# Kernel tuning notes

Measured on AMD Instinct MI355X. Metric: run time of the kernel, lower is better.

Reference implementation:

```python
import jax, jax.numpy as jnp
import numpy as np

EPS = 1e-5

def layernorm(x, g, b):
    mu = jnp.mean(x, axis=-1, keepdims=True)
    var = jnp.var(x, axis=-1, keepdims=True)
    return (x - mu) * jax.lax.rsqrt(var + EPS) * g + b

def setup_inputs() -> dict:
    key = jax.random.key(0)
    ks = jax.random.split(key, 12)
    B, T, C, H = 8, 2048, 64, 4
    d = C // H
    s = 0.02
    return {
        "x": jax.random.normal(ks[0], (B, T, C), jnp.float32),
        "Wq": jax.random.normal(ks[1], (H, C, d), jnp.float32) * s,
        "Wk": jax.random.normal(ks[2], (H, C, d), jnp.float32) * s,
        "Wv": jax.random.normal(ks[3], (H, C, d), jnp.float32) * s,
        "Wo": jax.random.normal(ks[4], (C, C), jnp.float32) * s,
        "bo": jnp.zeros((C,), jnp.float32),
        "W1": jax.random.normal(ks[5], (C, 4 * C), jnp.float32) * s,
        "bias1": jnp.zeros((4 * C,), jnp.float32),
        "W2": jax.random.normal(ks[6], (4 * C, C), jnp.float32) * s,
        "bias2": jnp.zeros((C,), jnp.float32),
        "gamma1": jnp.ones((C,), jnp.float32),
        "beta1": jnp.zeros((C,), jnp.float32),
        "gamma2": jnp.ones((C,), jnp.float32),
        "beta2": jnp.zeros((C,), jnp.float32),
    }

def reference(x, Wq, Wk, Wv, Wo, bo, W1, bias1, W2, bias2, gamma1, beta1, gamma2, beta2):
    B, T, C = x.shape
    H, _, d = Wq.shape
    # pre-LN attention
    h = layernorm(x, gamma1, beta1)
    q = jnp.einsum('btc,hcd->bhtd', h, Wq)
    k = jnp.einsum('btc,hcd->bhtd', h, Wk)
    v = jnp.einsum('btc,hcd->bhtd', h, Wv)
    scores = jnp.einsum('bhtd,bhsd->bhts', q, k) / jnp.sqrt(jnp.float32(d))
    causal = jnp.tril(jnp.ones((T, T), bool))
    scores = jnp.where(causal, scores, -jnp.inf)
    attn = jax.nn.softmax(scores, axis=-1)  # dropout = identity (eval)
    out = jnp.einsum('bhts,bhsd->bhtd', attn, v)
    out = out.transpose(0, 2, 1, 3).reshape(B, T, C)  # concat heads
    x = x + out @ Wo + bo
    # MLP
    h2 = layernorm(x, gamma2, beta2)
    x = x + jax.nn.relu(h2 @ W1 + bias1) @ W2 + bias2
    return x
```

## Files before the change

### kernel.cpp

```cpp
#include <hip/hip_runtime.h>

constexpr int Bn = 8, Tn = 2048;
constexpr int VS = 2080;

typedef __bf16 bf16x8 __attribute__((ext_vector_type(8)));
typedef float  f32x16 __attribute__((ext_vector_type(16)));
typedef short  short8 __attribute__((ext_vector_type(8)));
typedef unsigned short ushort_t;

__device__ __forceinline__ unsigned short f2bf(float f) {
    __bf16 h = (__bf16)f;
    return __builtin_bit_cast(unsigned short, h);
}

__device__ __forceinline__ float fast_exp2(float x) {
    float r;
    asm("v_exp_f32 %0, %1" : "=v"(r) : "v"(x));
    return r;
}

__device__ __forceinline__ unsigned cvt_pk_bf16(float lo, float hi_) {
    unsigned r;
    asm("v_cvt_pk_bf16_f32 %0, %1, %2" : "=v"(r) : "v"(lo), "v"(hi_));
    return r;
}

__device__ __forceinline__ bf16x8 xch_frag(
    float a0, float a1, float a2, float a3,
    float a4, float a5, float a6, float a7, int hi)
{
    const float s0 = hi ? a0 : a4, s1 = hi ? a1 : a5;
    const float s2 = hi ? a2 : a6, s3 = hi ? a3 : a7;
    const float r0 = __shfl_xor(s0, 32), r1 = __shfl_xor(s1, 32);
    const float r2 = __shfl_xor(s2, 32), r3 = __shfl_xor(s3, 32);
    bf16x8 f;
    f[0] = (__bf16)(hi ? r0 : a0); f[1] = (__bf16)(hi ? r1 : a1);
    f[2] = (__bf16)(hi ? r2 : a2); f[3] = (__bf16)(hi ? r3 : a3);
    f[4] = (__bf16)(hi ? a4 : r0); f[5] = (__bf16)(hi ? a5 : r1);
    f[6] = (__bf16)(hi ? a6 : r2); f[7] = (__bf16)(hi ? a7 : r3);
    return f;
}

__global__ __launch_bounds__(256) void k_prep(
    const float* __restrict__ Wo, const float* __restrict__ W1, const float* __restrict__ W2,
    const float* __restrict__ Wq, const float* __restrict__ Wk, const float* __restrict__ Wv,
    ushort_t* __restrict__ WoT, ushort_t* __restrict__ W1T, ushort_t* __restrict__ W2T,
    ushort_t* __restrict__ WqT, ushort_t* __restrict__ WkT, ushort_t* __restrict__ WvT,
    ushort_t* __restrict__ VT)
{
    const int i = blockIdx.x * 256 + threadIdx.x;
    if (i < 4096) {
        const int n = i >> 6, k = i & 63;
        WoT[i] = f2bf(Wo[k * 64 + n]);
    } else if (i < 20480) {
        const int i2 = i - 4096, n = i2 >> 6, k = i2 & 63;
        W1T[i2] = f2bf(W1[k * 256 + n]);
    } else if (i < 36864) {
        const int i2 = i - 20480, n = i2 >> 8, k = i2 & 255;
        W2T[i2] = f2bf(W2[k * 64 + n]);
    } else if (i < 49152) {
        const int j = i - 36864;
        const int a = j >> 12, jj = j & 4095;
        const int n = jj >> 6, c = jj & 63;
        const int src = (n >> 4) * 1024 + c * 16 + (n & 15);
        const float v = (a == 0) ? Wq[src] : (a == 1) ? Wk[src] : Wv[src];
        ushort_t* dst = (a == 0) ? WqT : (a == 1) ? WkT : WvT;
        dst[jj] = f2bf(v);
    } else if (i < 114688) {
        const int j = i - 49152;
        const int bh = j >> 11, t = j & 2047;
        VT[((size_t)bh * 32 + 16) * VS + t] = 0x3F80;
    }
}

__global__ __launch_bounds__(128) void k_ln_qkv(
    const float* __restrict__ x,
    const ushort_t* __restrict__ WqT, const ushort_t* __restrict__ WkT,
    const ushort_t* __restrict__ WvT,
    const float* __restrict__ g1, const float* __restrict__ b1,
    ushort_t* __restrict__ Qb, ushort_t* __restrict__ Kb, ushort_t* __restrict__ VT)
{
    __shared__ ushort_t wl0[64 * 64], wl1[64 * 64], wl2[64 * 64];
    const int tid = threadIdx.x;
    #pragma unroll
    for (int it = 0; it < 4; ++it) {
        const int i = it * 128 + tid;
        const int r = i >> 3, c = i & 7;
        const int dst = r * 64 + ((c ^ (r & 7)) * 8);
        *(short8*)&wl0[dst] = *(const short8*)&WqT[i * 8];
        *(short8*)&wl1[dst] = *(const short8*)&WkT[i * 8];
        *(short8*)&wl2[dst] = *(const short8*)&WvT[i * 8];
    }
    __syncthreads();

    const int w = tid >> 6, lane = tid & 63;
    const int hi = lane >> 5, m31 = lane & 31;
    const int tok = blockIdx.x * 64 + w * 32 + m31;
    const int b = tok >> 11, t2 = tok & 2047;

    float xc[4][8];
    #pragma unroll
    for (int ks = 0; ks < 4; ++ks) {
        const float4 u0 = *(const float4*)(x + (size_t)tok * 64 + 16 * ks + 8 * hi);
        const float4 u1 = *(const float4*)(x + (size_t)tok * 64 + 16 * ks + 8 * hi + 4);
        xc[ks][0] = u0.x; xc[ks][1] = u0.y; xc[ks][2] = u0.z; xc[ks][3] = u0.w;
        xc[ks][4] = u1.x; xc[ks][5] = u1.y; xc[ks][6] = u1.z; xc[ks][7] = u1.w;
    }
    float s = 0.f, sq = 0.f;
    #pragma unroll
    for (int ks = 0; ks < 4; ++ks)
        #pragma unroll
        for (int e = 0; e < 8; ++e) { s += xc[ks][e]; sq += xc[ks][e] * xc[ks][e]; }
    s  += __shfl_xor(s,  32);
    sq += __shfl_xor(sq, 32);
    const float mu  = s * (1.f / 64.f);
    const float var = sq * (1.f / 64.f) - mu * mu;
    const float rs  = rsqrtf(var + 1e-5f);

    bf16x8 hf[4];
    #pragma unroll
    for (int ks = 0; ks < 4; ++ks) {
        const float4 gq0 = *(const float4*)(g1 + 16 * ks + 8 * hi);
        const float4 gq1 = *(const float4*)(g1 + 16 * ks + 8 * hi + 4);
        const float4 bq0 = *(const float4*)(b1 + 16 * ks + 8 * hi);
        const float4 bq1 = *(const float4*)(b1 + 16 * ks + 8 * hi + 4);
        hf[ks][0] = (__bf16)((xc[ks][0] - mu) * rs * gq0.x + bq0.x);
        hf[ks][1] = (__bf16)((xc[ks][1] - mu) * rs * gq0.y + bq0.y);
        hf[ks][2] = (__bf16)((xc[ks][2] - mu) * rs * gq0.z + bq0.z);
        hf[ks][3] = (__bf16)((xc[ks][3] - mu) * rs * gq0.w + bq0.w);
        hf[ks][4] = (__bf16)((xc[ks][4] - mu) * rs * gq1.x + bq1.x);
        hf[ks][5] = (__bf16)((xc[ks][5] - mu) * rs * gq1.y + bq1.y);
        hf[ks][6] = (__bf16)((xc[ks][6] - mu) * rs * gq1.z + bq1.z);
        hf[ks][7] = (__bf16)((xc[ks][7] - mu) * rs * gq1.w + bq1.w);
    }

    f32x16 q0 = {}, q1 = {}, k0 = {}, k1 = {}, v0 = {}, v1 = {};
    #pragma unroll
    for (int ks = 0; ks < 4; ++ks) {
        const int ch = 2 * ks + hi;
        const int r0 = m31, r1 = m31 + 32;
        const bf16x8 aq0 = *(const bf16x8*)&wl0[r0 * 64 + ((ch ^ (r0 & 7)) * 8)];
        const bf16x8 aq1 = *(const bf16x8*)&wl0[r1 * 64 + ((ch ^ (r1 & 7)) * 8)];
        const bf16x8 ak0 = *(const bf16x8*)&wl1[r0 * 64 + ((ch ^ (r0 & 7)) * 8)];
        const bf16x8 ak1 = *(const bf16x8*)&wl1[r1 * 64 + ((ch ^ (r1 & 7)) * 8)];
        const bf16x8 av0 = *(const bf16x8*)&wl2[r0 * 64 + ((ch ^ (r0 & 7)) * 8)];
        const bf16x8 av1 = *(const bf16x8*)&wl2[r1 * 64 + ((ch ^ (r1 & 7)) * 8)];
        q0 = __builtin_amdgcn_mfma_f32_32x32x16_bf16(aq0, hf[ks], q0, 0, 0, 0);
        q1 = __builtin_amdgcn_mfma_f32_32x32x16_bf16(aq1, hf[ks], q1, 0, 0, 0);
        k0 = __builtin_amdgcn_mfma_f32_32x32x16_bf16(ak0, hf[ks], k0, 0, 0, 0);
        k1 = __builtin_amdgcn_mfma_f32_32x32x16_bf16(ak1, hf[ks], k1, 0, 0, 0);
        v0 = __builtin_amdgcn_mfma_f32_32x32x16_bf16(av0, hf[ks], v0, 0, 0, 0);
        v1 = __builtin_amdgcn_mfma_f32_32x32x16_bf16(av1, hf[ks], v1, 0, 0, 0);
    }

    const float SC = 0.360673760222f;
    #pragma unroll
    for (int nt = 0; nt < 2; ++nt) {
        const f32x16& qa = nt ? q1 : q0;
        const f32x16& ka = nt ? k1 : k0;
        const f32x16& va = nt ? v1 : v0;
        #pragma unroll
        for (int qd = 0; qd < 4; ++qd) {
            const int hd0 = 8 * qd + 4 * hi + 32 * nt;
            const int hh = hd0 >> 4, d0 = hd0 & 15;
            const int r0 = 4 * qd;
            const size_t off = ((size_t)(b * 4 + hh) * Tn + t2) * 16 + d0;
            uint2 uq, uk;
            uq.x = cvt_pk_bf16(qa[r0] * SC,  qa[r0+1] * SC);
            uq.y = cvt_pk_bf16(qa[r0+2] * SC, qa[r0+3] * SC);
            uk.x = cvt_pk_bf16(ka[r0],  ka[r0+1]);
            uk.y = cvt_pk_bf16(ka[r0+2], ka[r0+3]);
            *(uint2*)(Qb + off) = uq;
            *(uint2*)(Kb + off) = uk;
        }
        #pragma unroll
        for (int r = 0; r < 16; ++r) {
            const int hd = (r & 3) + 8 * (r >> 2) + 4 * hi + 32 * nt;
            const int hh = hd >> 4, d = hd & 15;
            VT[((size_t)(b * 4 + hh) * 32 + d) * VS + t2] = f2bf(va[r]);
        }
    }
}

#define ATTN_TILE(KF, V0, V1, KT)                                               \
    {                                                                           \
        f32x16 cinit;                                                           \
        _Pragma("unroll")                                                       \
        for (int r = 0; r < 16; ++r) cinit[r] = -m;                             \
        f32x16 st = __builtin_amdgcn_mfma_f32_32x32x16_bf16(KF, qf, cinit, 0, 0, 0); \
        if ((KT) == qt) {                                                       \
            _Pragma("unroll")                                                   \
            for (int r = 0; r < 16; ++r) {                                      \
                const int kr = (r & 3) + 8 * (r >> 2) + 4 * hi;                 \
                if (kr > qcol) st[r] = -30000.f;                                \
            }                                                                   \
        }                                                                       \
        float tm = fmaxf(fmaxf(fmaxf(st[0], st[1]),  fmaxf(st[2],  st[3])),     \
                         fmaxf(fmaxf(st[4], st[5]),  fmaxf(st[6],  st[7])));    \
        tm = fmaxf(tm,                                                          \
             fmaxf(fmaxf(fmaxf(st[8], st[9]),  fmaxf(st[10], st[11])),          \
                   fmaxf(fmaxf(st[12], st[13]), fmaxf(st[14], st[15]))));       \
        if (!__all(tm <= 0.f)) {                                                \
            float tm2 = fmaxf(tm, __shfl_xor(tm, 32));                          \
            tm2 = fmaxf(tm2, 0.f);                                              \
            const float corr = fast_exp2(-tm2);                                 \
            m += tm2;                                                           \
            _Pragma("unroll")                                                   \
            for (int r = 0; r < 9; ++r) oacc[r] *= corr;                        \
            _Pragma("unroll")                                                   \
            for (int r = 0; r < 16; ++r) st[r] -= tm2;                          \
        }                                                                       \
        float p[16];                                                            \
        _Pragma("unroll")                                                       \
        for (int r = 0; r < 16; ++r) p[r] = fast_exp2(st[r]);                   \
        const unsigned w0 = cvt_pk_bf16(p[0],  p[1]),  w1 = cvt_pk_bf16(p[2],  p[3]); \
        const unsigned w2 = cvt_pk_bf16(p[4],  p[5]),  w3 = cvt_pk_bf16(p[6],  p[7]); \
        const unsigned w4 = cvt_pk_bf16(p[8],  p[9]),  w5 = cvt_pk_bf16(p[10], p[11]); \
        const unsigned w6 = cvt_pk_bf16(p[12], p[13]), w7 = cvt_pk_bf16(p[14], p[15]); \
        const unsigned r0 = __shfl_xor(hi ? w0 : w2, 32);                       \
        const unsigned r1 = __shfl_xor(hi ? w1 : w3, 32);                       \
        const unsigned r2 = __shfl_xor(hi ? w4 : w6, 32);                       \
        const unsigned r3 = __shfl_xor(hi ? w5 : w7, 32);                       \
        union { unsigned u[4]; bf16x8 v; } pa0, pa1;                            \
        pa0.u[0] = hi ? r0 : w0;  pa0.u[1] = hi ? r1 : w1;                      \
        pa0.u[2] = hi ? w2 : r0;  pa0.u[3] = hi ? w3 : r1;                      \
        pa1.u[0] = hi ? r2 : w4;  pa1.u[1] = hi ? r3 : w5;                      \
        pa1.u[2] = hi ? w6 : r2;  pa1.u[3] = hi ? w7 : r3;                      \
        oacc = __builtin_amdgcn_mfma_f32_32x32x16_bf16(V0, pa0.v, oacc, 0, 0, 0); \
        oacc = __builtin_amdgcn_mfma_f32_32x32x16_bf16(V1, pa1.v, oacc, 0, 0, 0); \
    }

__global__ __launch_bounds__(256) void k_attn(
    const ushort_t* __restrict__ Qb, const ushort_t* __restrict__ Kb,
    const ushort_t* __restrict__ VT, ushort_t* __restrict__ AOb)
{
    const int wave = threadIdx.x >> 6, lane = threadIdx.x & 63;
    const int xcd = blockIdx.x & 7;
    const int q_  = blockIdx.x >> 3;
    const int bh  = xcd * 4 + (q_ >> 5);
    const int qtA = q_ & 31;
    const int w = wave;
    const int hi = lane >> 5, qcol = lane & 31;
    const int b = bh >> 2, h = bh & 3;

    const int vrow_i = (lane & 31) > 16 ? 16 : (lane & 31);
    const ushort_t* Qbh = Qb + (size_t)bh * (Tn * 16);
    const ushort_t* kaddr = Kb + (size_t)bh * (Tn * 16) + (size_t)qcol * 16 + 8 * hi;
    const ushort_t* vaddr = VT + (size_t)bh * (32 * VS) + (size_t)vrow_i * VS + 8 * hi;

    __shared__ float red[4][2][64][12];

    for (int rep = 0; rep < 2; ++rep) {
        const int qt = rep ? (63 - qtA) : qtA;

        const bf16x8 qf = *(const bf16x8*)(Qbh + (size_t)(qt * 32 + qcol) * 16 + 8 * hi);

        float m = 12.0f;
        f32x16 oacc = {};

        if (w <= qt) {
            const int ktB0 = (w + 4 <= qt) ? (w + 4) : qt;
            bf16x8 kfA = *(const bf16x8*)(kaddr + (size_t)w * 512);
            bf16x8 v0A = *(const bf16x8*)(vaddr + w * 32);
            bf16x8 v1A = *(const bf16x8*)(vaddr + w * 32 + 16);
            bf16x8 kfB = *(const bf16x8*)(kaddr + (size_t)ktB0 * 512);
            bf16x8 v0B = *(const bf16x8*)(vaddr + ktB0 * 32);
            bf16x8 v1B = *(const bf16x8*)(vaddr + ktB0 * 32 + 16);

            for (int kt = w; kt <= qt; kt += 8) {
                ATTN_TILE(kfA, v0A, v1A, kt);
                {
                    const int ktn = (kt + 8 <= qt) ? (kt + 8) : qt;
                    kfA = *(const bf16x8*)(kaddr + (size_t)ktn * 512);
                    v0A = *(const bf16x8*)(vaddr + ktn * 32);
                    v1A = *(const bf16x8*)(vaddr + ktn * 32 + 16);
                }
                if (kt + 4 <= qt) {
                    ATTN_TILE(kfB, v0B, v1B, kt + 4);
                    const int ktn = (kt + 12 <= qt) ? (kt + 12) : qt;
                    kfB = *(const bf16x8*)(kaddr + (size_t)ktn * 512);
                    v0B = *(const bf16x8*)(vaddr + ktn * 32);
                    v1B = *(const bf16x8*)(vaddr + ktn * 32 + 16);
                }
            }
        }

        const float lo_ = __shfl_xor(oacc[8], 32);
        const float l = hi ? lo_ : oacc[8];

        float* sp = &red[wave][rep][lane][0];
        sp[0] = m; sp[1] = l;
        #pragma unroll
        for (int r = 0; r < 8; ++r) sp[2 + r] = oacc[r];
    }
    __syncthreads();

    if (wave < 2) {
        const int r_m = wave;
        const float* p0 = &red[0][r_m][lane][0];
        const float* p1 = &red[1][r_m][lane][0];
        const float* p2 = &red[2][r_m][lane][0];
        const float* p3 = &red[3][r_m][lane][0];
        const float mm = fmaxf(fmaxf(p0[0], p1[0]), fmaxf(p2[0], p3[0]));
        const float c0 = fast_exp2(p0[0] - mm), c1 = fast_exp2(p1[0] - mm);
        const float c2 = fast_exp2(p2[0] - mm), c3 = fast_exp2(p3[0] - mm);
        const float lt = fmaf(p0[1], c0, fmaf(p1[1], c1, fmaf(p2[1], c2, p3[1] * c3)));
        const float inv = 1.f / lt;

        const int qt_out = r_m ? (63 - qtA) : qtA;
        const int qg2 = qt_out * 32 + qcol;

        float o[8];
        #pragma unroll
        for (int r = 0; r < 8; ++r)
            o[r] = fmaf(p0[2 + r], c0, fmaf(p1[2 + r], c1,
                   fmaf(p2[2 + r], c2, p3[2 + r] * c3))) * inv;

        ushort_t* dst = AOb + ((size_t)b * Tn + qg2) * 64 + h * 16;
        ushort4 u0, u1;
        u0.x = f2bf(o[0]); u0.y = f2bf(o[1]); u0.z = f2bf(o[2]); u0.w = f2bf(o[3]);
        u1.x = f2bf(o[4]); u1.y = f2bf(o[5]); u1.z = f2bf(o[6]); u1.w = f2bf(o[7]);
        *(ushort4*)(dst + 4 * hi)     = u0;
        *(ushort4*)(dst + 8 + 4 * hi) = u1;
    }
}

__global__ __launch_bounds__(128) void k_mlp(
    const float* __restrict__ x, const ushort_t* __restrict__ AOb,
    const ushort_t* __restrict__ WoTg, const float* __restrict__ bo,
    const float* __restrict__ g2, const float* __restrict__ b2v,
    const ushort_t* __restrict__ W1Tg, const float* __restrict__ bias1,
    const ushort_t* __restrict__ W2Tg, const float* __restrict__ bias2,
    float* __restrict__ out)
{
    __shared__ ushort_t wo_l[64 * 64];
    __shared__ ushort_t w1_l[256 * 64];
    __shared__ ushort_t w2_l[64 * 256];
    const int tid = threadIdx.x;
    #pragma unroll
    for (int it = 0; it < 4; ++it) {
        const int i = it * 128 + tid;
        const int r = i >> 3, c = i & 7;
        *(short8*)&wo_l[r * 64 + ((c ^ (r & 7)) * 8)] = *(const short8*)&WoTg[i * 8];
    }
    #pragma unroll
    for (int it = 0; it < 16; ++it) {
        const int i = it * 128 + tid;
        const int r = i >> 3, c = i & 7;
        *(short8*)&w1_l[r * 64 + ((c ^ (r & 7)) * 8)] = *(const short8*)&W1Tg[i * 8];
    }
    #pragma unroll
    for (int it = 0; it < 16; ++it) {
        const int i = it * 128 + tid;
        const int r = i >> 5, c = i & 31;
        *(short8*)&w2_l[r * 256 + ((c ^ (r & 7)) * 8)] = *(const short8*)&W2Tg[i * 8];
    }
    __syncthreads();

    const int w = tid >> 6, lane = tid & 63;
    const int hi = lane >> 5, m31 = lane & 31;
    const size_t m = (size_t)(blockIdx.x * 2 + w) * 32 + m31;

    f32x16 y0 = {}, y1 = {};
    {
        const ushort_t* ar = AOb + m * 64 + 8 * hi;
        const int r0 = m31, r1 = m31 + 32;
        #pragma unroll
        for (int ks = 0; ks < 4; ++ks) {
            const int ch = 2 * ks + hi;
            const bf16x8 bf = *(const bf16x8*)(ar + 16 * ks);
            const bf16x8 a0 = *(const bf16x8*)&wo_l[r0 * 64 + ((ch ^ (r0 & 7)) * 8)];
            const bf16x8 a1 = *(const bf16x8*)&wo_l[r1 * 64 + ((ch ^ (r1 & 7)) * 8)];
            y0 = __builtin_amdgcn_mfma_f32_32x32x16_bf16(a0, bf, y0, 0, 0, 0);
            y1 = __builtin_amdgcn_mfma_f32_32x32x16_bf16(a1, bf, y1, 0, 0, 0);
        }
    }

    #pragma unroll
    for (int q2 = 0; q2 < 4; ++q2) {
        {
            const int nb = 8 * q2 + 4 * hi;
            const float4 xq = *(const float4*)(x + m * 64 + nb);
            const float4 bq = *(const float4*)(bo + nb);
            y0[4*q2+0] += xq.x + bq.x; y0[4*q2+1] += xq.y + bq.y;
            y0[4*q2+2] += xq.z + bq.z; y0[4*q2+3] += xq.w + bq.w;
        }
        {
            const int nb = 32 + 8 * q2 + 4 * hi;
            const float4 xq = *(const float4*)(x + m * 64 + nb);
            const float4 bq = *(const float4*)(bo + nb);
            y1[4*q2+0] += xq.x + bq.x; y1[4*q2+1] += xq.y + bq.y;
            y1[4*q2+2] += xq.z + bq.z; y1[4*q2+3] += xq.w + bq.w;
        }
    }

    float s = 0.f, sq = 0.f;
    #pragma unroll
    for (int r = 0; r < 16; ++r) {
        s  += y0[r] + y1[r];
        sq += y0[r] * y0[r] + y1[r] * y1[r];
    }
    s  += __shfl_xor(s,  32);
    sq += __shfl_xor(sq, 32);
    const float mu  = s * (1.f / 64.f);
    const float var = sq * (1.f / 64.f) - mu * mu;
    const float rs  = rsqrtf(var + 1e-5f);

    float hreg[32];
    #pragma unroll
    for (int q2 = 0; q2 < 4; ++q2) {
        {
            const int nb = 8 * q2 + 4 * hi;
            const float4 gq = *(const float4*)(g2 + nb);
            const float4 bq = *(const float4*)(b2v + nb);
            hreg[4*q2+0] = (y0[4*q2+0] - mu) * rs * gq.x + bq.x;
            hreg[4*q2+1] = (y0[4*q2+1] - mu) * rs * gq.y + bq.y;
            hreg[4*q2+2] = (y0[4*q2+2] - mu) * rs * gq.z + bq.z;
            hreg[4*q2+3] = (y0[4*q2+3] - mu) * rs * gq.w + bq.w;
        }
        {
            const int nb = 32 + 8 * q2 + 4 * hi;
            const float4 gq = *(const float4*)(g2 + nb);
            const float4 bq = *(const float4*)(b2v + nb);
            hreg[16+4*q2+0] = (y1[4*q2+0] - mu) * rs * gq.x + bq.x;
            hreg[16+4*q2+1] = (y1[4*q2+1] - mu) * rs * gq.y + bq.y;
            hreg[16+4*q2+2] = (y1[4*q2+2] - mu) * rs * gq.z + bq.z;
            hreg[16+4*q2+3] = (y1[4*q2+3] - mu) * rs * gq.w + bq.w;
        }
    }

    f32x16 o0 = {}, o1 = {};
    #pragma unroll
    for (int g = 0; g < 8; ++g) {
        f32x16 hacc = {};
        #pragma unroll
        for (int ks = 0; ks < 4; ++ks) {
            const int base = 16 * (ks >> 1) + 8 * (ks & 1);
            const bf16x8 bf = xch_frag(hreg[base+0], hreg[base+1], hreg[base+2], hreg[base+3],
                                       hreg[base+4], hreg[base+5], hreg[base+6], hreg[base+7], hi);
            const int rw = 32 * g + m31;
            const int ch = 2 * ks + hi;
            const bf16x8 a = *(const bf16x8*)&w1_l[rw * 64 + ((ch ^ (rw & 7)) * 8)];
            hacc = __builtin_amdgcn_mfma_f32_32x32x16_bf16(a, bf, hacc, 0, 0, 0);
        }
        float hv[16];
        #pragma unroll
        for (int q2 = 0; q2 < 4; ++q2) {
            const int nb = 32 * g + 8 * q2 + 4 * hi;
            const float4 bq = *(const float4*)(bias1 + nb);
            hv[4*q2+0] = fmaxf(hacc[4*q2+0] + bq.x, 0.f);
            hv[4*q2+1] = fmaxf(hacc[4*q2+1] + bq.y, 0.f);
            hv[4*q2+2] = fmaxf(hacc[4*q2+2] + bq.z, 0.f);
            hv[4*q2+3] = fmaxf(hacc[4*q2+3] + bq.w, 0.f);
        }
        #pragma unroll
        for (int w2 = 0; w2 < 2; ++w2) {
            const int base = 8 * w2;
            const bf16x8 bf = xch_frag(hv[base+0], hv[base+1], hv[base+2], hv[base+3],
                                       hv[base+4], hv[base+5], hv[base+6], hv[base+7], hi);
            const int ch = 4 * g + 2 * w2 + hi;
            const int r0 = m31, r1 = m31 + 32;
            const bf16x8 a0 = *(const bf16x8*)&w2_l[r0 * 256 + ((ch ^ (r0 & 7)) * 8)];
            const bf16x8 a1 = *(const bf16x8*)&w2_l[r1 * 256 + ((ch ^ (r1 & 7)) * 8)];
            o0 = __builtin_amdgcn_mfma_f32_32x32x16_bf16(a0, bf, o0, 0, 0, 0);
            o1 = __builtin_amdgcn_mfma_f32_32x32x16_bf16(a1, bf, o1, 0, 0, 0);
        }
    }

    #pragma unroll
    for (int q2 = 0; q2 < 4; ++q2) {
        {
            const int nb = 8 * q2 + 4 * hi;
            const float4 bq = *(const float4*)(bias2 + nb);
            float4 r;
            r.x = y0[4*q2+0] + o0[4*q2+0] + bq.x;
            r.y = y0[4*q2+1] + o0[4*q2+1] + bq.y;
            r.z = y0[4*q2+2] + o0[4*q2+2] + bq.z;
            r.w = y0[4*q2+3] + o0[4*q2+3] + bq.w;
            *(float4*)(out + m * 64 + nb) = r;
        }
        {
            const int nb = 32 + 8 * q2 + 4 * hi;
            const float4 bq = *(const float4*)(bias2 + nb);
            float4 r;
            r.x = y1[4*q2+0] + o1[4*q2+0] + bq.x;
            r.y = y1[4*q2+1] + o1[4*q2+1] + bq.y;
            r.z = y1[4*q2+2] + o1[4*q2+2] + bq.z;
            r.w = y1[4*q2+3] + o1[4*q2+3] + bq.w;
            *(float4*)(out + m * 64 + nb) = r;
        }
    }
}

extern "C" void kernel_launch(void* const* d_in, const int* in_sizes, int n_in,
                              void* d_out, int out_size, void* d_ws, size_t ws_size,
                              hipStream_t stream)
{
    const float* x     = (const float*)d_in[0];
    const float* Wq    = (const float*)d_in[1];
    const float* Wk    = (const float*)d_in[2];
    const float* Wv    = (const float*)d_in[3];
    const float* Wo    = (const float*)d_in[4];
    const float* bo    = (const float*)d_in[5];
    const float* W1    = (const float*)d_in[6];
    const float* bias1 = (const float*)d_in[7];
    const float* W2    = (const float*)d_in[8];
    const float* bias2 = (const float*)d_in[9];
    const float* g1    = (const float*)d_in[10];
    const float* be1   = (const float*)d_in[11];
    const float* g2    = (const float*)d_in[12];
    const float* be2   = (const float*)d_in[13];

    const size_t nBF = (size_t)32 * Tn * 16;
    ushort_t* Qb  = (ushort_t*)d_ws;
    ushort_t* Kb  = Qb + nBF;
    ushort_t* VT  = Kb + nBF;
    ushort_t* AOb = VT + (size_t)32 * 32 * VS;
    ushort_t* WoT = AOb + nBF;
    ushort_t* W1T = WoT + 4096;
    ushort_t* W2T = W1T + 16384;
    ushort_t* WqT = W2T + 16384;
    ushort_t* WkT = WqT + 4096;
    ushort_t* WvT = WkT + 4096;

    k_prep<<<dim3(448), dim3(256), 0, stream>>>(Wo, W1, W2, Wq, Wk, Wv,
                                                WoT, W1T, W2T, WqT, WkT, WvT, VT);
    k_ln_qkv<<<dim3((Bn * Tn) / 64), dim3(128), 0, stream>>>(
        x, WqT, WkT, WvT, g1, be1, Qb, Kb, VT);
    k_attn<<<dim3(32 * 32), dim3(256), 0, stream>>>(Qb, Kb, VT, AOb);
    k_mlp<<<dim3((Bn * Tn) / 64), dim3(128), 0, stream>>>(
        x, AOb, WoT, bo, g2, be2, W1T, bias1, W2T, bias2, (float*)d_out);
}
```

Before: 46.00 us.

## Split QKV and MLP work across twice the waves per block

k_ln_qkv and k_mlp now launch 256 threads per block, with two waves per 32-token tile. In k_ln_qkv each wave computes half the output features, so each wave does fewer MFMAs and holds fewer accumulators. In k_mlp each wave handles half of the hidden groups and the partial W2 outputs are reduced through shared memory. The ones-column write into VT moves from k_prep into k_ln_qkv, which shrinks the prep grid. The aim is more parallelism and shorter per-wave critical paths, at the cost of redundant LayerNorm and attention-output-projection work per wave pair plus an extra barrier and LDS reduction in the MLP.

```diff
diff --git a/kernel.cpp b/kernel.cpp
--- a/kernel.cpp
+++ b/kernel.cpp
@@ -45,8 +45,7 @@
     const float* __restrict__ Wo, const float* __restrict__ W1, const float* __restrict__ W2,
     const float* __restrict__ Wq, const float* __restrict__ Wk, const float* __restrict__ Wv,
     ushort_t* __restrict__ WoT, ushort_t* __restrict__ W1T, ushort_t* __restrict__ W2T,
-    ushort_t* __restrict__ WqT, ushort_t* __restrict__ WkT, ushort_t* __restrict__ WvT,
-    ushort_t* __restrict__ VT)
+    ushort_t* __restrict__ WqT, ushort_t* __restrict__ WkT, ushort_t* __restrict__ WvT)
 {
     const int i = blockIdx.x * 256 + threadIdx.x;
     if (i < 4096) {
@@ -66,14 +65,10 @@
         const float v = (a == 0) ? Wq[src] : (a == 1) ? Wk[src] : Wv[src];
         ushort_t* dst = (a == 0) ? WqT : (a == 1) ? WkT : WvT;
         dst[jj] = f2bf(v);
-    } else if (i < 114688) {
-        const int j = i - 49152;
-        const int bh = j >> 11, t = j & 2047;
-        VT[((size_t)bh * 32 + 16) * VS + t] = 0x3F80;
-    }
-}
-
-__global__ __launch_bounds__(128) void k_ln_qkv(
+    }
+}
+
+__global__ __launch_bounds__(256) void k_ln_qkv(
     const float* __restrict__ x,
     const ushort_t* __restrict__ WqT, const ushort_t* __restrict__ WkT,
     const ushort_t* __restrict__ WvT,
@@ -83,8 +78,8 @@
     __shared__ ushort_t wl0[64 * 64], wl1[64 * 64], wl2[64 * 64];
     const int tid = threadIdx.x;
     #pragma unroll
-    for (int it = 0; it < 4; ++it) {
-        const int i = it * 128 + tid;
+    for (int it = 0; it < 2; ++it) {
+        const int i = it * 256 + tid;
         const int r = i >> 3, c = i & 7;
         const int dst = r * 64 + ((c ^ (r & 7)) * 8);
         *(short8*)&wl0[dst] = *(const short8*)&WqT[i * 8];
@@ -93,9 +88,10 @@
     }
     __syncthreads();
 
-    const int w = tid >> 6, lane = tid & 63;
+    const int wave = tid >> 6, lane = tid & 63;
+    const int tile = wave >> 1, u = wave & 1;
     const int hi = lane >> 5, m31 = lane & 31;
-    const int tok = blockIdx.x * 64 + w * 32 + m31;
+    const int tok = blockIdx.x * 64 + tile * 32 + m31;
     const int b = tok >> 11, t2 = tok & 2047;
 
     float xc[4][8];
@@ -134,51 +130,45 @@
         hf[ks][7] = (__bf16)((xc[ks][7] - mu) * rs * gq1.w + bq1.w);
     }
 
-    f32x16 q0 = {}, q1 = {}, k0 = {}, k1 = {}, v0 = {}, v1 = {};
+    f32x16 q = {}, k = {}, v = {};
+    const int rw = m31 + 32 * u;
     #pragma unroll
     for (int ks = 0; ks < 4; ++ks) {
         const int ch = 2 * ks + hi;
-        const int r0 = m31, r1 = m31 + 32;
-        const bf16x8 aq0 = *(const bf16x8*)&wl0[r0 * 64 + ((ch ^ (r0 & 7)) * 8)];
-        const bf16x8 aq1 = *(const bf16x8*)&wl0[r1 * 64 + ((ch ^ (r1 & 7)) * 8)];
-        const bf16x8 ak0 = *(const bf16x8*)&wl1[r0 * 64 + ((ch ^ (r0 & 7)) * 8)];
-        const bf16x8 ak1 = *(const bf16x8*)&wl1[r1 * 64 + ((ch ^ (r1 & 7)) * 8)];
-        const bf16x8 av0 = *(const bf16x8*)&wl2[r0 * 64 + ((ch ^ (r0 & 7)) * 8)];
-        const bf16x8 av1 = *(const bf16x8*)&wl2[r1 * 64 + ((ch ^ (r1 & 7)) * 8)];
-        q0 = __builtin_amdgcn_mfma_f32_32x32x16_bf16(aq0, hf[ks], q0, 0, 0, 0);
-        q1 = __builtin_amdgcn_mfma_f32_32x32x16_bf16(aq1, hf[ks], q1, 0, 0, 0);
-        k0 = __builtin_amdgcn_mfma_f32_32x32x16_bf16(ak0, hf[ks], k0, 0, 0, 0);
-        k1 = __builtin_amdgcn_mfma_f32_32x32x16_bf16(ak1, hf[ks], k1, 0, 0, 0);
-        v0 = __builtin_amdgcn_mfma_f32_32x32x16_bf16(av0, hf[ks], v0, 0, 0, 0);
-        v1 = __builtin_amdgcn_mfma_f32_32x32x16_bf16(av1, hf[ks], v1, 0, 0, 0);
+        const int wo = rw * 64 + ((ch ^ (rw & 7)) * 8);
+        const bf16x8 aq = *(const bf16x8*)&wl0[wo];
+        const bf16x8 ak = *(const bf16x8*)&wl1[wo];
+        const bf16x8 av = *(const bf16x8*)&wl2[wo];
+        q = __builtin_amdgcn_mfma_f32_32x32x16_bf16(aq, hf[ks], q, 0, 0, 0);
+        k = __builtin_amdgcn_mfma_f32_32x32x16_bf16(ak, hf[ks], k, 0, 0, 0);
+        v = __builtin_amdgcn_mfma_f32_32x32x16_bf16(av, hf[ks], v, 0, 0, 0);
     }
 
     const float SC = 0.360673760222f;
     #pragma unroll
-    for (int nt = 0; nt < 2; ++nt) {
-        const f32x16& qa = nt ? q1 : q0;
-        const f32x16& ka = nt ? k1 : k0;
-        const f32x16& va = nt ? v1 : v0;
-        #pragma unroll
-        for (int qd = 0; qd < 4; ++qd) {
-            const int hd0 = 8 * qd + 4 * hi + 32 * nt;
-            const int hh = hd0 >> 4, d0 = hd0 & 15;
-            const int r0 = 4 * qd;
-            const size_t off = ((size_t)(b * 4 + hh) * Tn + t2) * 16 + d0;
-            uint2 uq, uk;
-            uq.x = cvt_pk_bf16(qa[r0] * SC,  qa[r0+1] * SC);
-            uq.y = cvt_pk_bf16(qa[r0+2] * SC, qa[r0+3] * SC);
-            uk.x = cvt_pk_bf16(ka[r0],  ka[r0+1]);
-            uk.y = cvt_pk_bf16(ka[r0+2], ka[r0+3]);
-            *(uint2*)(Qb + off) = uq;
-            *(uint2*)(Kb + off) = uk;
-        }
-        #pragma unroll
-        for (int r = 0; r < 16; ++r) {
-            const int hd = (r & 3) + 8 * (r >> 2) + 4 * hi + 32 * nt;
-            const int hh = hd >> 4, d = hd & 15;
-            VT[((size_t)(b * 4 + hh) * 32 + d) * VS + t2] = f2bf(va[r]);
-        }
+    for (int qd = 0; qd < 4; ++qd) {
+        const int hd0 = 8 * qd + 4 * hi + 32 * u;
+        const int hh = hd0 >> 4, d0 = hd0 & 15;
+        const int r0 = 4 * qd;
+        const size_t off = ((size_t)(b * 4 + hh) * Tn + t2) * 16 + d0;
+        uint2 uq, uk;
+        uq.x = cvt_pk_bf16(q[r0] * SC,   q[r0+1] * SC);
+        uq.y = cvt_pk_bf16(q[r0+2] * SC, q[r0+3] * SC);
+        uk.x = cvt_pk_bf16(k[r0],  k[r0+1]);
+        uk.y = cvt_pk_bf16(k[r0+2], k[r0+3]);
+        *(uint2*)(Qb + off) = uq;
+        *(uint2*)(Kb + off) = uk;
+    }
+    #pragma unroll
+    for (int r = 0; r < 16; ++r) {
+        const int hd = (r & 3) + 8 * (r >> 2) + 4 * hi + 32 * u;
+        const int hh = hd >> 4, d = hd & 15;
+        VT[((size_t)(b * 4 + hh) * 32 + d) * VS + t2] = f2bf(v[r]);
+    }
+    if (u == 0) {
+        #pragma unroll
+        for (int hh = 0; hh < 4; ++hh)
+            VT[((size_t)(b * 4 + hh) * 32 + 16) * VS + t2] = 0x3F80;
     }
 }
 
@@ -325,7 +315,7 @@
     }
 }
 
-__global__ __launch_bounds__(128) void k_mlp(
+__global__ __launch_bounds__(256) void k_mlp(
     const float* __restrict__ x, const ushort_t* __restrict__ AOb,
     const ushort_t* __restrict__ WoTg, const float* __restrict__ bo,
     const float* __restrict__ g2, const float* __restrict__ b2v,
@@ -336,30 +326,32 @@
     __shared__ ushort_t wo_l[64 * 64];
     __shared__ ushort_t w1_l[256 * 64];
     __shared__ ushort_t w2_l[64 * 256];
+    __shared__ float part[2][64][34];
     const int tid = threadIdx.x;
     #pragma unroll
-    for (int it = 0; it < 4; ++it) {
-        const int i = it * 128 + tid;
+    for (int it = 0; it < 2; ++it) {
+        const int i = it * 256 + tid;
         const int r = i >> 3, c = i & 7;
         *(short8*)&wo_l[r * 64 + ((c ^ (r & 7)) * 8)] = *(const short8*)&WoTg[i * 8];
     }
     #pragma unroll
-    for (int it = 0; it < 16; ++it) {
-        const int i = it * 128 + tid;
+    for (int it = 0; it < 8; ++it) {
+        const int i = it * 256 + tid;
         const int r = i >> 3, c = i & 7;
         *(short8*)&w1_l[r * 64 + ((c ^ (r & 7)) * 8)] = *(const short8*)&W1Tg[i * 8];
     }
     #pragma unroll
-    for (int it = 0; it < 16; ++it) {
-        const int i = it * 128 + tid;
+    for (int it = 0; it < 8; ++it) {
+        const int i = it * 256 + tid;
         const int r = i >> 5, c = i & 31;
         *(short8*)&w2_l[r * 256 + ((c ^ (r & 7)) * 8)] = *(const short8*)&W2Tg[i * 8];
     }
     __syncthreads();
 
-    const int w = tid >> 6, lane = tid & 63;
+    const int wave = tid >> 6, lane = tid & 63;
+    const int tile = wave >> 1, u = wave & 1;
     const int hi = lane >> 5, m31 = lane & 31;
-    const size_t m = (size_t)(blockIdx.x * 2 + w) * 32 + m31;
+    const size_t m = (size_t)(blockIdx.x * 2 + tile) * 32 + m31;
 
     f32x16 y0 = {}, y1 = {};
     {
@@ -431,7 +423,8 @@
 
     f32x16 o0 = {}, o1 = {};
     #pragma unroll
-    for (int g = 0; g < 8; ++g) {
+    for (int gi = 0; gi < 4; ++gi) {
+        const int g = 4 * u + gi;
         f32x16 hacc = {};
         #pragma unroll
         for (int ks = 0; ks < 4; ++ks) {
@@ -467,27 +460,44 @@
         }
     }
 
-    #pragma unroll
-    for (int q2 = 0; q2 < 4; ++q2) {
-        {
-            const int nb = 8 * q2 + 4 * hi;
-            const float4 bq = *(const float4*)(bias2 + nb);
-            float4 r;
-            r.x = y0[4*q2+0] + o0[4*q2+0] + bq.x;
-            r.y = y0[4*q2+1] + o0[4*q2+1] + bq.y;
-            r.z = y0[4*q2+2] + o0[4*q2+2] + bq.z;
-            r.w = y0[4*q2+3] + o0[4*q2+3] + bq.w;
-            *(float4*)(out + m * 64 + nb) = r;
-        }
-        {
-            const int nb = 32 + 8 * q2 + 4 * hi;
-            const float4 bq = *(const float4*)(bias2 + nb);
-            float4 r;
-            r.x = y1[4*q2+0] + o1[4*q2+0] + bq.x;
-            r.y = y1[4*q2+1] + o1[4*q2+1] + bq.y;
-            r.z = y1[4*q2+2] + o1[4*q2+2] + bq.z;
-            r.w = y1[4*q2+3] + o1[4*q2+3] + bq.w;
-            *(float4*)(out + m * 64 + nb) = r;
+    if (u == 1) {
+        #pragma unroll
+        for (int j = 0; j < 8; ++j) {
+            float2 a = make_float2(o0[2*j], o0[2*j+1]);
+            float2 bb = make_float2(o1[2*j], o1[2*j+1]);
+            *(float2*)&part[tile][lane][2*j]      = a;
+            *(float2*)&part[tile][lane][16 + 2*j] = bb;
+        }
+    }
+    __syncthreads();
+    if (u == 0) {
+        #pragma unroll
+        for (int r = 0; r < 16; ++r) {
+            o0[r] += part[tile][lane][r];
+            o1[r] += part[tile][lane][16 + r];
+        }
+        #pragma unroll
+        for (int q2 = 0; q2 < 4; ++q2) {
+            {
+                const int nb = 8 * q2 + 4 * hi;
+                const float4 bq = *(const float4*)(bias2 + nb);
+                float4 r;
+                r.x = y0[4*q2+0] + o0[4*q2+0] + bq.x;
+                r.y = y0[4*q2+1] + o0[4*q2+1] + bq.y;
+                r.z = y0[4*q2+2] + o0[4*q2+2] + bq.z;
+                r.w = y0[4*q2+3] + o0[4*q2+3] + bq.w;
+                *(float4*)(out + m * 64 + nb) = r;
+            }
+            {
+                const int nb = 32 + 8 * q2 + 4 * hi;
+                const float4 bq = *(const float4*)(bias2 + nb);
+                float4 r;
+                r.x = y1[4*q2+0] + o1[4*q2+0] + bq.x;
+                r.y = y1[4*q2+1] + o1[4*q2+1] + bq.y;
+                r.z = y1[4*q2+2] + o1[4*q2+2] + bq.z;
+                r.w = y1[4*q2+3] + o1[4*q2+3] + bq.w;
+                *(float4*)(out + m * 64 + nb) = r;
+            }
         }
     }
 }
@@ -523,11 +533,11 @@
     ushort_t* WkT = WqT + 4096;
     ushort_t* WvT = WkT + 4096;
 
-    k_prep<<<dim3(448), dim3(256), 0, stream>>>(Wo, W1, W2, Wq, Wk, Wv,
-                                                WoT, W1T, W2T, WqT, WkT, WvT, VT);
-    k_ln_qkv<<<dim3((Bn * Tn) / 64), dim3(128), 0, stream>>>(
+    k_prep<<<dim3(192), dim3(256), 0, stream>>>(Wo, W1, W2, Wq, Wk, Wv,
+                                                WoT, W1T, W2T, WqT, WkT, WvT);
+    k_ln_qkv<<<dim3((Bn * Tn) / 64), dim3(256), 0, stream>>>(
         x, WqT, WkT, WvT, g1, be1, Qb, Kb, VT);
     k_attn<<<dim3(32 * 32), dim3(256), 0, stream>>>(Qb, Kb, VT, AOb);
-    k_mlp<<<dim3((Bn * Tn) / 64), dim3(128), 0, stream>>>(
+    k_mlp<<<dim3((Bn * Tn) / 64), dim3(256), 0, stream>>>(
         x, AOb, WoT, bo, g2, be2, W1T, bias1, W2T, bias2, (float*)d_out);
 }
```

Result: no change. 46.29 us (+0.6%).
